# Performance work log

Hardware: AMD Instinct MI355X
Metric: run time of the kernel (lower is better)

The kernel has to match this reference:

```python
import jax, jax.numpy as jnp
import numpy as np
import math

B, S, T = 64, 512, 512
N, F_NODE, F_TRIP = 2000, 128, 128
D, H, GD = 512, 8, 64  # concat fusion: D == H*GD
SECONDS_PER_DAY = 3600.0 * 24.0


def cyclical_feat(t, mask):
    # t,[B,L]; mask,[B,L] -> [B,L,2]  (matches tf concat of sin/cos on axis 2)
    ang = 2.0 * math.pi * t / SECONDS_PER_DAY
    return jnp.stack([jnp.sin(ang) * mask, jnp.cos(ang) * mask], axis=-1)


def gat(x, adj, W, a_src, a_dst):
    # GAT-style AttentionAggregator, concat fusion + relu activation.
    # x:[N,F], adj:[N,N] (0/1), W:[H,F,G], a_src/a_dst:[H,G]
    h = jnp.einsum('nf,hfg->hng', x, W)                      # [H,N,G]
    es = jnp.einsum('hng,hg->hn', h, a_src)                  # [H,N]
    ed = jnp.einsum('hng,hg->hn', h, a_dst)                  # [H,N]
    e = jax.nn.leaky_relu(es[:, :, None] + ed[:, None, :], 0.2)  # [H,N,N]
    e = jnp.where(adj[None, :, :] > 0, e, -1e9)
    attn = jax.nn.softmax(e, axis=-1)                        # [H,N,N]
    out = jnp.einsum('hij,hjg->hig', attn, h)                # [H,N,G]
    out = jnp.transpose(out, (1, 0, 2)).reshape(x.shape[0], -1)  # [N,H*G]
    return jax.nn.relu(out)


def reconstruct_from_graph(graph_emb, index_array):
    # Vectorized equivalent of the TF TensorArray loop: indices are 1-based
    # with 0 = pad; valid entries are left-compacted, so masked gather == 
    # boolean_mask + gather + right-pad.
    valid = index_array > 0                                   # [B,S]
    idx = jnp.maximum(index_array - 1, 0)                     # [B,S]
    return jnp.where(valid[..., None], graph_emb[idx], 0.0)   # [B,S,D]


def setup_inputs() -> dict:
    key = jax.random.key(0)
    ks = jax.random.split(key, 13)
    region_batch = jax.random.normal(ks[0], (N, F_NODE), jnp.float32)
    trip_batch = jax.random.normal(ks[1], (B, T, F_TRIP), jnp.float32)
    len_r = jax.random.randint(ks[2], (B,), S // 2, S + 1)
    len_t = jax.random.randint(ks[3], (B,), T // 2, T + 1)
    region_mask = (jnp.arange(S)[None, :] < len_r[:, None]).astype(jnp.float32)
    trip_mask = (jnp.arange(T)[None, :] < len_t[:, None]).astype(jnp.float32)
    graph_mask = (jax.random.uniform(ks[4], (N, N)) < 0.02).astype(jnp.float32)
    graph_mask = jnp.maximum(graph_mask, jnp.eye(N, dtype=jnp.float32))  # self loops
    index_array = jax.random.randint(ks[5], (B, S), 1, N + 1).astype(jnp.int32)
    index_array = index_array * region_mask.astype(jnp.int32)  # 0 = pad (right side)
    arrive = jax.random.uniform(ks[6], (B, S), jnp.float32, 0.0, SECONDS_PER_DAY)
    depart = jax.random.uniform(ks[7], (B, T), jnp.float32, 0.0, SECONDS_PER_DAY)
    W_trip = jax.random.normal(ks[8], (F_TRIP, D), jnp.float32) * 0.05
    W_gat = jax.random.normal(ks[9], (H, F_NODE, GD), jnp.float32) * 0.05
    a_src = jax.random.normal(ks[10], (H, GD), jnp.float32) * 0.05
    a_dst = jax.random.normal(ks[11], (H, GD), jnp.float32) * 0.05
    W_time = jax.random.normal(ks[12], (2, D), jnp.float32) * 0.05
    b_time = jnp.zeros((D,), jnp.float32)
    return dict(region_batch=region_batch, trip_batch=trip_batch,
                trip_mask=trip_mask, region_mask=region_mask, graph_mask=graph_mask,
                arrive=arrive, depart=depart, index_array=index_array,
                W_trip=W_trip, W_gat=W_gat, a_src=a_src, a_dst=a_dst,
                W_time=W_time, b_time=b_time)


def reference(region_batch, trip_batch, trip_mask, region_mask, graph_mask,
              arrive, depart, index_array, W_trip, W_gat, a_src, a_dst,
              W_time, b_time):
    # FeatureExtractionLayer assumed Dense(no bias) + relu; dropout=0 (eval).
    trip_embeddings = jax.nn.relu(jnp.einsum('btf,fd->btd', trip_batch, W_trip))
    graph_embeddings = gat(region_batch, graph_mask, W_gat, a_src, a_dst)  # [N,D]
    region_embeddings = reconstruct_from_graph(graph_embeddings, index_array)
    arrive_feat = cyclical_feat(arrive, region_mask)   # [B,S,2]
    depart_feat = cyclical_feat(depart, trip_mask)     # [B,T,2]
    region_embeddings = region_embeddings + arrive_feat @ W_time + b_time
    trip_embeddings = trip_embeddings + depart_feat @ W_time + b_time
    return (region_embeddings, trip_embeddings)
```

## Files before the change

kernel.cpp:

```cpp
#include <hip/hip_runtime.h>
#include <hip/hip_bf16.h>

#define NB 2000
#define FN 128
#define DD 512
#define HH 8
#define GG 64
#define BB 64
#define SS 512
#define TT 512

__device__ __forceinline__ bool is_bf16(const void* graph_mask) {
    return (((const unsigned*)graph_mask)[0] & 0xFFFFu) == 0x3F80u;
}

template<bool BF>
__device__ __forceinline__ float ld(const void* p, long i) {
    if constexpr (BF) return __bfloat162float(((const __hip_bfloat16*)p)[i]);
    else              return ((const float*)p)[i];
}
template<bool BF>
__device__ __forceinline__ void st(void* p, long i, float v) {
    if constexpr (BF) ((__hip_bfloat16*)p)[i] = __float2bfloat16(v);
    else              ((float*)p)[i] = v;
}

template<bool BF>
__device__ __forceinline__ void ld4(const void* p, long i, float* o) {
    if constexpr (BF) {
        const unsigned short* q = (const unsigned short*)p + i;
        uint2 v = *reinterpret_cast<const uint2*>(q);
        o[0] = __uint_as_float((v.x & 0xFFFFu) << 16);
        o[1] = __uint_as_float((v.x >> 16) << 16);
        o[2] = __uint_as_float((v.y & 0xFFFFu) << 16);
        o[3] = __uint_as_float((v.y >> 16) << 16);
    } else {
        float4 a = *reinterpret_cast<const float4*>((const float*)p + i);
        o[0]=a.x; o[1]=a.y; o[2]=a.z; o[3]=a.w;
    }
}
template<bool BF>
__device__ __forceinline__ void ld8(const void* p, long i, float* o) {
    if constexpr (BF) {
        const unsigned short* q = (const unsigned short*)p + i;
        uint4 v = *reinterpret_cast<const uint4*>(q);
        unsigned a0 = v.x, a1 = v.y, a2 = v.z, a3 = v.w;
        o[0] = __uint_as_float((a0 & 0xFFFFu) << 16);
        o[1] = __uint_as_float((a0 >> 16) << 16);
        o[2] = __uint_as_float((a1 & 0xFFFFu) << 16);
        o[3] = __uint_as_float((a1 >> 16) << 16);
        o[4] = __uint_as_float((a2 & 0xFFFFu) << 16);
        o[5] = __uint_as_float((a2 >> 16) << 16);
        o[6] = __uint_as_float((a3 & 0xFFFFu) << 16);
        o[7] = __uint_as_float((a3 >> 16) << 16);
    } else {
        const float* q = (const float*)p + i;
        float4 a = *reinterpret_cast<const float4*>(q);
        float4 b = *reinterpret_cast<const float4*>(q + 4);
        o[0]=a.x; o[1]=a.y; o[2]=a.z; o[3]=a.w;
        o[4]=b.x; o[5]=b.y; o[6]=b.z; o[7]=b.w;
    }
}
__device__ __forceinline__ unsigned pack_bf2(float a, float b) {
    __hip_bfloat16 x = __float2bfloat16(a), y = __float2bfloat16(b);
    return (unsigned)*(unsigned short*)&x | ((unsigned)*(unsigned short*)&y << 16);
}
template<bool BF>
__device__ __forceinline__ void st8(void* p, long i, const float* v) {
    if constexpr (BF) {
        unsigned short* q = (unsigned short*)p + i;
        *reinterpret_cast<uint4*>(q) = make_uint4(
            pack_bf2(v[0], v[1]), pack_bf2(v[2], v[3]),
            pack_bf2(v[4], v[5]), pack_bf2(v[6], v[7]));
    } else {
        float* q = (float*)p + i;
        *reinterpret_cast<float4*>(q)     = make_float4(v[0],v[1],v[2],v[3]);
        *reinterpret_cast<float4*>(q + 4) = make_float4(v[4],v[5],v[6],v[7]);
    }
}

__device__ __forceinline__ unsigned short f2bf(float v) {
    __hip_bfloat16 h = __float2bfloat16(v);
    return *reinterpret_cast<unsigned short*>(&h);
}
__device__ __forceinline__ float bf2f(unsigned short s) {
    return __uint_as_float((unsigned)s << 16);
}

#define NPB 8

template<bool BF>
__device__ __forceinline__ void gat_h_body(
    const void* __restrict__ x, const void* __restrict__ Wg,
    const void* __restrict__ a_src, const void* __restrict__ a_dst,
    float* __restrict__ h_ws, float* __restrict__ es_ws, float* __restrict__ ed_ws,
    float (*__restrict__ xs)[FN])
{
    int n0  = blockIdx.x * NPB;
    int tid = threadIdx.x;
    int hh  = tid >> 5, gp = tid & 31;
    int g0  = gp * 2;

    if constexpr (BF) {
        for (int idx = tid; idx < NPB * FN / 8; idx += 256) {
            float o[8];
            ld8<BF>(x, (long)n0 * FN + idx * 8, o);
#pragma unroll
            for (int j = 0; j < 8; ++j) ((float*)xs)[idx * 8 + j] = o[j];
        }
    } else {
        const float4* src = (const float4*)((const float*)x + (long)n0 * FN);
        for (int idx = tid; idx < NPB * FN / 4; idx += 256)
            ((float4*)xs)[idx] = src[idx];
    }
    __syncthreads();

    float v0[NPB], v1[NPB];
#pragma unroll
    for (int nn = 0; nn < NPB; ++nn) { v0[nn] = 0.f; v1[nn] = 0.f; }

    if constexpr (BF) {
        const unsigned* wp = (const unsigned*)((const unsigned short*)Wg + (long)hh * FN * GG);
#pragma unroll 4
        for (int f = 0; f < FN; ++f) {
            unsigned w = wp[f * 32 + gp];
            float wx = __uint_as_float((w & 0xFFFFu) << 16);
            float wy = __uint_as_float((w >> 16) << 16);
#pragma unroll
            for (int nn = 0; nn < NPB; ++nn) {
                float xf = xs[nn][f];
                v0[nn] = fmaf(xf, wx, v0[nn]);
                v1[nn] = fmaf(xf, wy, v1[nn]);
            }
        }
    } else {
        const float2* wp = (const float2*)((const float*)Wg + (long)hh * FN * GG);
#pragma unroll 4
        for (int f = 0; f < FN; ++f) {
            float2 w = wp[f * 32 + gp];
#pragma unroll
            for (int nn = 0; nn < NPB; ++nn) {
                float xf = xs[nn][f];
                v0[nn] = fmaf(xf, w.x, v0[nn]);
                v1[nn] = fmaf(xf, w.y, v1[nn]);
            }
        }
    }

    float as0 = ld<BF>(a_src, hh * GG + g0), as1 = ld<BF>(a_src, hh * GG + g0 + 1);
    float ad0 = ld<BF>(a_dst, hh * GG + g0), ad1 = ld<BF>(a_dst, hh * GG + g0 + 1);
#pragma unroll
    for (int nn = 0; nn < NPB; ++nn) {
        int n = n0 + nn;
        *reinterpret_cast<float2*>(&h_ws[((long)hh * NB + n) * GG + g0]) =
            make_float2(v0[nn], v1[nn]);
        float s1 = v0[nn] * as0 + v1[nn] * as1;
        float s2 = v0[nn] * ad0 + v1[nn] * ad1;
        for (int off = 16; off > 0; off >>= 1) {
            s1 += __shfl_xor(s1, off);
            s2 += __shfl_xor(s2, off);
        }
        if (gp == 0) { es_ws[hh * NB + n] = s1; ed_ws[hh * NB + n] = s2; }
    }
}

__global__ __launch_bounds__(256) void gat_h_kernel(
    const void* x, const void* Wg, const void* a_src, const void* a_dst,
    float* h_ws, float* es_ws, float* ed_ws, const void* graph_mask)
{
    __shared__ float xs[NPB][FN];
    if (is_bf16(graph_mask)) gat_h_body<true >(x, Wg, a_src, a_dst, h_ws, es_ws, ed_ws, xs);
    else                     gat_h_body<false>(x, Wg, a_src, a_dst, h_ws, es_ws, ed_ws, xs);
}

#define ACAP 192

template<bool BF>
__device__ __forceinline__ void gat_attn_body(
    const void* __restrict__ adj,
    const float* __restrict__ h_ws, const float* __restrict__ es_ws,
    const float* __restrict__ ed_ws, float* __restrict__ ge_ws,
    int* __restrict__ jl, float (*__restrict__ wts)[ACAP],
    float* __restrict__ es_i, int* __restrict__ cnt)
{
    const int i    = blockIdx.x;
    const int tid  = threadIdx.x;
    const int w    = tid >> 6;
    const int lane = tid & 63;

    if (tid == 0) *cnt = 0;
    if (tid < HH) es_i[tid] = es_ws[tid * NB + i];
    __syncthreads();

    for (int base = w * 64; base < NB; base += 512) {
        int  j     = base + lane;
        bool valid = (j < NB) && (ld<BF>(adj, (long)i * NB + j) > 0.f);
        unsigned long long mask = __ballot(valid);
        int nv = __popcll(mask);
        int bs = 0;
        if (lane == 0 && nv) bs = atomicAdd(cnt, nv);
        bs = __shfl(bs, 0);
        if (valid) {
            int slot = bs + __popcll(mask & ((1ULL << lane) - 1ULL));
            jl[slot] = j;
        }
    }
    __syncthreads();
    const int cn = min(*cnt, ACAP);

    const float es = es_i[w];
    float e_r[3];
    float m = -INFINITY;
#pragma unroll
    for (int s = 0; s < 3; ++s) {
        int k = lane + s * 64;
        float e = -INFINITY;
        if (k < cn) {
            float ev = es + ed_ws[(long)w * NB + jl[k]];
            e = ev > 0.f ? ev : 0.2f * ev;
        }
        e_r[s] = e;
        m = fmaxf(m, e);
    }
    for (int off = 32; off > 0; off >>= 1) m = fmaxf(m, __shfl_xor(m, off));
    float l = 0.f;
#pragma unroll
    for (int s = 0; s < 3; ++s) {
        int k = lane + s * 64;
        if (k < cn) {
            float p = __expf(e_r[s] - m);
            wts[w][k] = p;
            l += p;
        }
    }
    for (int off = 32; off > 0; off >>= 1) l += __shfl_xor(l, off);

    const float* hp = h_ws + (long)w * NB * GG + lane;
    float acc = 0.f;
    int k = 0;
    for (; k + 4 <= cn; k += 4) {
        float e0 = wts[w][k],   e1 = wts[w][k+1];
        float e2 = wts[w][k+2], e3 = wts[w][k+3];
        int   j0 = jl[k],   j1 = jl[k+1], j2 = jl[k+2], j3 = jl[k+3];
        float h0 = hp[(long)j0 * GG];
        float h1 = hp[(long)j1 * GG];
        float h2 = hp[(long)j2 * GG];
        float h3 = hp[(long)j3 * GG];
        acc = fmaf(e3, h3, fmaf(e2, h2, fmaf(e1, h1, fmaf(e0, h0, acc))));
    }
    for (; k < cn; ++k)
        acc = fmaf(wts[w][k], hp[(long)jl[k] * GG], acc);

    ge_ws[(long)i * DD + w * GG + lane] = fmaxf(acc / l, 0.f);
}

__global__ __launch_bounds__(512) void gat_attn_kernel(
    const void* adj, const float* h_ws, const float* es_ws,
    const float* ed_ws, float* ge_ws)
{
    __shared__ int   jl[2048];
    __shared__ float wts[HH][ACAP];
    __shared__ float es_i[HH];
    __shared__ int   cnt;
    if (is_bf16(adj)) gat_attn_body<true >(adj, h_ws, es_ws, ed_ws, ge_ws, jl, wts, es_i, &cnt);
    else              gat_attn_body<false>(adj, h_ws, es_ws, ed_ws, ge_ws, jl, wts, es_i, &cnt);
}

template<bool BF>
__device__ __forceinline__ void region_out_body(
    const int* __restrict__ index_array, const void* __restrict__ arrive,
    const void* __restrict__ region_mask,
    const void* __restrict__ W_time, const void* __restrict__ b_time,
    const float* __restrict__ ge_ws, void* __restrict__ out)
{
    int row  = blockIdx.x * 4 + (threadIdx.x >> 6);
    int lane = threadIdx.x & 63;
    int d0   = lane * 8;
    int idx  = index_array[row];
    float mask = ld<BF>(region_mask, row);
    float t    = ld<BF>(arrive, row);
    float ang  = 6.28318530717958647692f * t / 86400.f;
    float sa = sinf(ang) * mask, ca = cosf(ang) * mask;
    float g[8] = {0.f,0.f,0.f,0.f,0.f,0.f,0.f,0.f};
    if (idx > 0) {
        const float* gp = ge_ws + (long)(idx - 1) * DD + d0;
        float4 a = *reinterpret_cast<const float4*>(gp);
        float4 b = *reinterpret_cast<const float4*>(gp + 4);
        g[0]=a.x; g[1]=a.y; g[2]=a.z; g[3]=a.w;
        g[4]=b.x; g[5]=b.y; g[6]=b.z; g[7]=b.w;
    }
    float wt0[8], wt1[8], bt[8], o[8];
    ld8<BF>(W_time, d0, wt0);
    ld8<BF>(W_time, DD + d0, wt1);
    ld8<BF>(b_time, d0, bt);
#pragma unroll
    for (int j = 0; j < 8; ++j)
        o[j] = g[j] + sa * wt0[j] + ca * wt1[j] + bt[j];
    st8<BF>(out, (long)row * DD + d0, o);
}

__global__ __launch_bounds__(256) void region_out_kernel(
    const int* index_array, const void* arrive, const void* region_mask,
    const void* W_time, const void* b_time, const float* ge_ws, void* out,
    const void* graph_mask)
{
    if (is_bf16(graph_mask))
        region_out_body<true >(index_array, arrive, region_mask, W_time, b_time, ge_ws, out);
    else
        region_out_body<false>(index_array, arrive, region_mask, W_time, b_time, ge_ws, out);
}

typedef __attribute__((ext_vector_type(8))) short bf16x8;
typedef __attribute__((ext_vector_type(4))) float f32x4;

#define MFMA_BF16 __builtin_amdgcn_mfma_f32_16x16x32_bf16

__global__ __launch_bounds__(256) void prep_x_kernel(
    const void* __restrict__ trip_batch, unsigned short* __restrict__ Xh_p,
    unsigned short* __restrict__ Xl_p, const void* graph_mask)
{
    if (is_bf16(graph_mask)) return;
    long i = ((long)blockIdx.x * 256 + threadIdx.x) * 8;
    const float* q = (const float*)trip_batch + i;
    float4 a = *reinterpret_cast<const float4*>(q);
    float4 b = *reinterpret_cast<const float4*>(q + 4);
    float v[8] = {a.x,a.y,a.z,a.w,b.x,b.y,b.z,b.w};
    unsigned short h[8], l[8];
#pragma unroll
    for (int j = 0; j < 8; ++j) {
        h[j] = f2bf(v[j]);
        l[j] = f2bf(v[j] - bf2f(h[j]));
    }
    *reinterpret_cast<uint4*>(Xh_p + i) = make_uint4(
        h[0] | ((unsigned)h[1] << 16), h[2] | ((unsigned)h[3] << 16),
        h[4] | ((unsigned)h[5] << 16), h[6] | ((unsigned)h[7] << 16));
    *reinterpret_cast<uint4*>(Xl_p + i) = make_uint4(
        l[0] | ((unsigned)l[1] << 16), l[2] | ((unsigned)l[3] << 16),
        l[4] | ((unsigned)l[5] << 16), l[6] | ((unsigned)l[7] << 16));
}

__global__ __launch_bounds__(256) void prep_w_kernel(
    const void* __restrict__ W_trip, unsigned short* __restrict__ Wh_p,
    unsigned short* __restrict__ Wl_p, const void* graph_mask)
{
    bool bf = is_bf16(graph_mask);
    int q  = blockIdx.x * 256 + threadIdx.x;
    int k  = q >> 7;
    int n0 = (q & 127) * 4;
    if (bf) {
        const unsigned short* w = (const unsigned short*)W_trip;
#pragma unroll
        for (int j = 0; j < 4; ++j)
            Wh_p[(n0 + j) * FN + k] = w[(long)k * DD + n0 + j];
    } else {
        float v[4];
        ld4<false>(W_trip, (long)k * DD + n0, v);
#pragma unroll
        for (int j = 0; j < 4; ++j) {
            unsigned short h = f2bf(v[j]);
            Wh_p[(n0 + j) * FN + k] = h;
            Wl_p[(n0 + j) * FN + k] = f2bf(v[j] - bf2f(h));
        }
    }
}

template<bool BF>
__device__ __forceinline__ void trip_gemm_body(
    const unsigned short* __restrict__ Xh_p, const unsigned short* __restrict__ Xl_p,
    const unsigned short* __restrict__ Wh_p, const unsigned short* __restrict__ Wl_p,
    const void* __restrict__ depart, const void* __restrict__ trip_mask,
    const void* __restrict__ W_time, const void* __restrict__ b_time,
    void* __restrict__ out,
    short* __restrict__ Xh, short* __restrict__ Xl,
    short* __restrict__ Wh, short* __restrict__ Wl)
{
    const int tid  = threadIdx.x;
    const int lane = tid & 63;
    const int wv   = tid >> 6;
    const int bx   = blockIdx.x & 7;
    const int by   = blockIdx.x >> 3;
    const int row0 = by * 64;
    const int c0   = bx * 64;

    f32x4 acc0 = {0.f,0.f,0.f,0.f}, acc1 = {0.f,0.f,0.f,0.f};
    f32x4 acc2 = {0.f,0.f,0.f,0.f}, acc3 = {0.f,0.f,0.f,0.f};

    const int mr  = wv * 16 + (lane & 15);
    const int nrb = lane & 15;
    const int kl  = (lane >> 4) * 8;

    for (int kh = 0; kh < 2; ++kh) {
        if (kh) __syncthreads();

        for (int q = tid; q < 512; q += 256) {
            int r  = q >> 3, k8 = q & 7;
            long src = (long)(row0 + r) * FN + kh * 64 + k8 * 8;
            int  dst = r * 64 + ((k8 * 8) ^ ((r & 7) << 3));
            *reinterpret_cast<uint4*>(&Xh[dst]) =
                *reinterpret_cast<const uint4*>(Xh_p + src);
            if constexpr (!BF)
                *reinterpret_cast<uint4*>(&Xl[dst]) =
                    *reinterpret_cast<const uint4*>(Xl_p + src);
        }
        for (int q = tid; q < 512; q += 256) {
            int n  = q >> 3, k8 = q & 7;
            long src = (long)(c0 + n) * FN + kh * 64 + k8 * 8;
            int  dst = n * 64 + ((k8 * 8) ^ ((n & 7) << 3));
            *reinterpret_cast<uint4*>(&Wh[dst]) =
                *reinterpret_cast<const uint4*>(Wh_p + src);
            if constexpr (!BF)
                *reinterpret_cast<uint4*>(&Wl[dst]) =
                    *reinterpret_cast<const uint4*>(Wl_p + src);
        }
        __syncthreads();

#pragma unroll
        for (int kc = 0; kc < 2; ++kc) {
            int k0 = kc * 32 + kl;
            int ax = mr * 64 + (k0 ^ ((mr & 7) << 3));
            bf16x8 ah = *reinterpret_cast<const bf16x8*>(&Xh[ax]);
            bf16x8 al;
            if constexpr (!BF) al = *reinterpret_cast<const bf16x8*>(&Xl[ax]);
#pragma unroll
            for (int nt = 0; nt < 4; ++nt) {
                int nr = nt * 16 + nrb, wi = nr * 64 + (k0 ^ ((nr & 7) << 3));
                bf16x8 bh = *reinterpret_cast<const bf16x8*>(&Wh[wi]);
                f32x4& acc = (nt == 0) ? acc0 : (nt == 1) ? acc1 : (nt == 2) ? acc2 : acc3;
                acc = MFMA_BF16(ah, bh, acc, 0, 0, 0);
                if constexpr (!BF) {
                    bf16x8 bl = *reinterpret_cast<const bf16x8*>(&Wl[wi]);
                    acc = MFMA_BF16(al, bh, acc, 0, 0, 0);
                    acc = MFMA_BF16(ah, bl, acc, 0, 0, 0);
                }
            }
        }
    }

    const int rbase = row0 + wv * 16 + (lane >> 4) * 4;
    float sa[4], ca[4];
#pragma unroll
    for (int r = 0; r < 4; ++r) {
        int   row  = rbase + r;
        float mask = ld<BF>(trip_mask, row);
        float t    = ld<BF>(depart, row);
        float ang  = 6.28318530717958647692f * t / 86400.f;
        sa[r] = sinf(ang) * mask;
        ca[r] = cosf(ang) * mask;
    }
    const long obase = (long)BB * SS * DD;
#pragma unroll
    for (int nt = 0; nt < 4; ++nt) {
        int   c   = c0 + nt * 16 + (lane & 15);
        float wt0 = ld<BF>(W_time, c);
        float wt1 = ld<BF>(W_time, DD + c);
        float bt  = ld<BF>(b_time, c);
        f32x4 a = (nt == 0) ? acc0 : (nt == 1) ? acc1 : (nt == 2) ? acc2 : acc3;
#pragma unroll
        for (int r = 0; r < 4; ++r) {
            float o = fmaxf(a[r], 0.f) + sa[r] * wt0 + ca[r] * wt1 + bt;
            st<BF>(out, obase + (long)(rbase + r) * DD + c, o);
        }
    }
}

__global__ __launch_bounds__(256) void trip_gemm_kernel(
    const void* trip_batch,
    const unsigned short* Xh_p, const unsigned short* Xl_p,
    const unsigned short* Wh_p, const unsigned short* Wl_p,
    const void* depart, const void* trip_mask,
    const void* W_time, const void* b_time, void* out, const void* graph_mask)
{
    __shared__ short Xh[64 * 64], Xl[64 * 64];
    __shared__ short Wh[64 * 64], Wl[64 * 64];
    if (is_bf16(graph_mask))
        trip_gemm_body<true >((const unsigned short*)trip_batch, Xl_p, Wh_p, Wl_p,
                              depart, trip_mask, W_time, b_time, out, Xh, Xl, Wh, Wl);
    else
        trip_gemm_body<false>(Xh_p, Xl_p, Wh_p, Wl_p,
                              depart, trip_mask, W_time, b_time, out, Xh, Xl, Wh, Wl);
}

template<bool BF>
__device__ __forceinline__ void trip_mfma_body(
    const void* __restrict__ trip_batch, const void* __restrict__ W_trip,
    const void* __restrict__ depart, const void* __restrict__ trip_mask,
    const void* __restrict__ W_time, const void* __restrict__ b_time,
    void* __restrict__ out,
    short* __restrict__ Xh, short* __restrict__ Xl,
    short* __restrict__ Wh, short* __restrict__ Wl)
{
    const int tid  = threadIdx.x;
    const int lane = tid & 63;
    const int wv   = tid >> 6;
    const int bx   = blockIdx.x & 7;
    const int by   = blockIdx.x >> 3;
    const int row0 = by * 64;
    const int c0   = bx * 64;

    f32x4 acc0 = {0.f,0.f,0.f,0.f}, acc1 = {0.f,0.f,0.f,0.f};
    f32x4 acc2 = {0.f,0.f,0.f,0.f}, acc3 = {0.f,0.f,0.f,0.f};

    const int mr  = wv * 16 + (lane & 15);
    const int nrb = lane & 15;
    const int kl  = (lane >> 4) * 8;

    for (int kh = 0; kh < 2; ++kh) {
        if (kh) __syncthreads();
        for (int q = tid; q < 1024; q += 256) {
            int r  = q >> 4;
            int k4 = (q & 15) * 4;
            float v[4];
            ld4<BF>(trip_batch, (long)(row0 + r) * FN + kh * 64 + k4, v);
            int base = r * 64 + (k4 ^ ((r & 7) << 3));
            ushort4 hs, ls;
            hs.x = f2bf(v[0]); ls.x = f2bf(v[0] - bf2f(hs.x));
            hs.y = f2bf(v[1]); ls.y = f2bf(v[1] - bf2f(hs.y));
            hs.z = f2bf(v[2]); ls.z = f2bf(v[2] - bf2f(hs.z));
            hs.w = f2bf(v[3]); ls.w = f2bf(v[3] - bf2f(hs.w));
            *reinterpret_cast<ushort4*>(&Xh[base]) = hs;
            *reinterpret_cast<ushort4*>(&Xl[base]) = ls;
        }
        for (int q = tid; q < 1024; q += 256) {
            int k  = q >> 4;
            int n0 = (q & 15) * 4;
            float v[4];
            ld4<BF>(W_trip, (long)(kh * 64 + k) * DD + c0 + n0, v);
#pragma unroll
            for (int j = 0; j < 4; ++j) {
                int n   = n0 + j;
                int idx = n * 64 + (k ^ ((n & 7) << 3));
                unsigned short h = f2bf(v[j]);
                Wh[idx] = (short)h;
                Wl[idx] = (short)f2bf(v[j] - bf2f(h));
            }
        }
        __syncthreads();

#pragma unroll
        for (int kc = 0; kc < 2; ++kc) {
            int k0 = kc * 32 + kl;
            int ax = mr * 64 + (k0 ^ ((mr & 7) << 3));
            bf16x8 ah = *reinterpret_cast<const bf16x8*>(&Xh[ax]);
            bf16x8 al = *reinterpret_cast<const bf16x8*>(&Xl[ax]);
#pragma unroll
            for (int nt = 0; nt < 4; ++nt) {
                int nr = nt * 16 + nrb, wi = nr * 64 + (k0 ^ ((nr & 7) << 3));
                bf16x8 bh = *reinterpret_cast<const bf16x8*>(&Wh[wi]);
                bf16x8 bl = *reinterpret_cast<const bf16x8*>(&Wl[wi]);
                f32x4& acc = (nt == 0) ? acc0 : (nt == 1) ? acc1 : (nt == 2) ? acc2 : acc3;
                acc = MFMA_BF16(ah, bh, acc, 0, 0, 0);
                acc = MFMA_BF16(al, bh, acc, 0, 0, 0);
                acc = MFMA_BF16(ah, bl, acc, 0, 0, 0);
            }
        }
    }

    const int rbase = row0 + wv * 16 + (lane >> 4) * 4;
    float sa[4], ca[4];
#pragma unroll
    for (int r = 0; r < 4; ++r) {
        int   row  = rbase + r;
        float mask = ld<BF>(trip_mask, row);
        float t    = ld<BF>(depart, row);
        float ang  = 6.28318530717958647692f * t / 86400.f;
        sa[r] = sinf(ang) * mask;
        ca[r] = cosf(ang) * mask;
    }
    const long obase = (long)BB * SS * DD;
#pragma unroll
    for (int nt = 0; nt < 4; ++nt) {
        int   c   = c0 + nt * 16 + (lane & 15);
        float wt0 = ld<BF>(W_time, c);
        float wt1 = ld<BF>(W_time, DD + c);
        float bt  = ld<BF>(b_time, c);
        f32x4 a = (nt == 0) ? acc0 : (nt == 1) ? acc1 : (nt == 2) ? acc2 : acc3;
#pragma unroll
        for (int r = 0; r < 4; ++r) {
            float o = fmaxf(a[r], 0.f) + sa[r] * wt0 + ca[r] * wt1 + bt;
            st<BF>(out, obase + (long)(rbase + r) * DD + c, o);
        }
    }
}

__global__ __launch_bounds__(256) void trip_out_kernel(
    const void* trip_batch, const void* W_trip, const void* depart,
    const void* trip_mask, const void* W_time, const void* b_time, void* out,
    const void* graph_mask)
{
    __shared__ short Xh[64 * 64], Xl[64 * 64];
    __shared__ short Wh[64 * 64], Wl[64 * 64];
    if (is_bf16(graph_mask))
        trip_mfma_body<true >(trip_batch, W_trip, depart, trip_mask, W_time, b_time, out, Xh, Xl, Wh, Wl);
    else
        trip_mfma_body<false>(trip_batch, W_trip, depart, trip_mask, W_time, b_time, out, Xh, Xl, Wh, Wl);
}

extern "C" void kernel_launch(void* const* d_in, const int* in_sizes, int n_in,
                              void* d_out, int out_size, void* d_ws, size_t ws_size,
                              hipStream_t stream) {
    const void* region_batch = d_in[0];
    const void* trip_batch   = d_in[1];
    const void* trip_mask    = d_in[2];
    const void* region_mask  = d_in[3];
    const void* graph_mask   = d_in[4];
    const void* arrive       = d_in[5];
    const void* depart       = d_in[6];
    const int*  index_array  = (const int*)d_in[7];
    const void* W_trip       = d_in[8];
    const void* W_gat        = d_in[9];
    const void* a_src        = d_in[10];
    const void* a_dst        = d_in[11];
    const void* W_time       = d_in[12];
    const void* b_time       = d_in[13];

    float* h_ws  = (float*)d_ws;
    float* es_ws = h_ws  + HH * NB * GG;
    float* ed_ws = es_ws + HH * NB;
    float* ge_ws = ed_ws + HH * NB;
    unsigned short* Xh_p = (unsigned short*)(ge_ws + (long)NB * DD);
    unsigned short* Xl_p = Xh_p + (long)BB * TT * FN;
    unsigned short* Wh_p = Xl_p + (long)BB * TT * FN;
    unsigned short* Wl_p = Wh_p + FN * DD;
    const size_t need = (size_t)((Wl_p + FN * DD) - (unsigned short*)d_ws) * 2;

    gat_h_kernel<<<NB / NPB, 256, 0, stream>>>(region_batch, W_gat, a_src, a_dst,
                                               h_ws, es_ws, ed_ws, graph_mask);
    gat_attn_kernel<<<NB, 512, 0, stream>>>(graph_mask, h_ws, es_ws, ed_ws, ge_ws);
    region_out_kernel<<<BB * SS / 4, 256, 0, stream>>>(index_array, arrive, region_mask,
                                                       W_time, b_time, ge_ws, d_out, graph_mask);
    if (ws_size >= need) {
        prep_x_kernel<<<(BB * TT * FN) / (256 * 8), 256, 0, stream>>>(
            trip_batch, Xh_p, Xl_p, graph_mask);
        prep_w_kernel<<<(FN * DD / 4) / 256, 256, 0, stream>>>(
            W_trip, Wh_p, Wl_p, graph_mask);
        trip_gemm_kernel<<<(BB * TT / 64) * (DD / 64), 256, 0, stream>>>(
            trip_batch, Xh_p, Xl_p, Wh_p, Wl_p,
            depart, trip_mask, W_time, b_time, d_out, graph_mask);
    } else {
        trip_out_kernel<<<(BB * TT / 64) * (DD / 64), 256, 0, stream>>>(
            trip_batch, W_trip, depart, trip_mask, W_time, b_time, d_out, graph_mask);
    }
}
```

Measured before the change: 269.8 us.

## Merge independent launches into combined front and tail kernels via block-range dispatch

Folds the GAT projection, the trip-input bf16 hi/lo split and the weight prep into one front kernel, with block index ranges choosing the role. The trip GEMM and the region gather/output are merged into one tail kernel in the same way, cutting six launches to three and letting independent work share the GPU. The adjacency scan in the attention kernel now issues all four row loads before doing the ballot compaction. The merged tail kernel reserves 32KB of LDS for every block, including the light region-output blocks, which may reduce their occupancy.

```diff
diff --git a/kernel.cpp b/kernel.cpp
--- a/kernel.cpp
+++ b/kernel.cpp
@@ -87,16 +87,21 @@
     return __uint_as_float((unsigned)s << 16);
 }
 
+typedef __attribute__((ext_vector_type(8))) short bf16x8;
+typedef __attribute__((ext_vector_type(4))) float f32x4;
+#define MFMA_BF16 __builtin_amdgcn_mfma_f32_16x16x32_bf16
+
 #define NPB 8
 
 template<bool BF>
 __device__ __forceinline__ void gat_h_body(
+    int blk,
     const void* __restrict__ x, const void* __restrict__ Wg,
     const void* __restrict__ a_src, const void* __restrict__ a_dst,
     float* __restrict__ h_ws, float* __restrict__ es_ws, float* __restrict__ ed_ws,
     float (*__restrict__ xs)[FN])
 {
-    int n0  = blockIdx.x * NPB;
+    int n0  = blk * NPB;
     int tid = threadIdx.x;
     int hh  = tid >> 5, gp = tid & 31;
     int g0  = gp * 2;
@@ -164,13 +169,75 @@
     }
 }
 
-__global__ __launch_bounds__(256) void gat_h_kernel(
-    const void* x, const void* Wg, const void* a_src, const void* a_dst,
-    float* h_ws, float* es_ws, float* ed_ws, const void* graph_mask)
+__device__ __forceinline__ void prep_x_body(
+    int blk, const void* __restrict__ trip_batch,
+    unsigned short* __restrict__ Xh_p, unsigned short* __restrict__ Xl_p)
+{
+    long i = ((long)blk * 256 + threadIdx.x) * 8;
+    const float* q = (const float*)trip_batch + i;
+    float4 a = *reinterpret_cast<const float4*>(q);
+    float4 b = *reinterpret_cast<const float4*>(q + 4);
+    float v[8] = {a.x,a.y,a.z,a.w,b.x,b.y,b.z,b.w};
+    unsigned short h[8], l[8];
+#pragma unroll
+    for (int j = 0; j < 8; ++j) {
+        h[j] = f2bf(v[j]);
+        l[j] = f2bf(v[j] - bf2f(h[j]));
+    }
+    *reinterpret_cast<uint4*>(Xh_p + i) = make_uint4(
+        h[0] | ((unsigned)h[1] << 16), h[2] | ((unsigned)h[3] << 16),
+        h[4] | ((unsigned)h[5] << 16), h[6] | ((unsigned)h[7] << 16));
+    *reinterpret_cast<uint4*>(Xl_p + i) = make_uint4(
+        l[0] | ((unsigned)l[1] << 16), l[2] | ((unsigned)l[3] << 16),
+        l[4] | ((unsigned)l[5] << 16), l[6] | ((unsigned)l[7] << 16));
+}
+
+__device__ __forceinline__ void prep_w_body(
+    int blk, bool bf, const void* __restrict__ W_trip,
+    unsigned short* __restrict__ Wh_p, unsigned short* __restrict__ Wl_p)
+{
+    int q  = blk * 256 + threadIdx.x;
+    int k  = q >> 7;
+    int n0 = (q & 127) * 4;
+    if (bf) {
+        const unsigned short* w = (const unsigned short*)W_trip;
+#pragma unroll
+        for (int j = 0; j < 4; ++j)
+            Wh_p[(n0 + j) * FN + k] = w[(long)k * DD + n0 + j];
+    } else {
+        float v[4];
+        ld4<false>(W_trip, (long)k * DD + n0, v);
+#pragma unroll
+        for (int j = 0; j < 4; ++j) {
+            unsigned short h = f2bf(v[j]);
+            Wh_p[(n0 + j) * FN + k] = h;
+            Wl_p[(n0 + j) * FN + k] = f2bf(v[j] - bf2f(h));
+        }
+    }
+}
+
+#define GATH_BLKS  (NB / NPB)
+#define PREPX_BLKS ((BB * TT * FN) / (256 * 8))
+#define PREPW_BLKS ((FN * DD / 4) / 256)
+
+__global__ __launch_bounds__(256) void front_kernel(
+    const void* region_batch, const void* Wg, const void* a_src, const void* a_dst,
+    float* h_ws, float* es_ws, float* ed_ws,
+    const void* trip_batch, unsigned short* Xh_p, unsigned short* Xl_p,
+    const void* W_trip, unsigned short* Wh_p, unsigned short* Wl_p,
+    const void* graph_mask)
 {
     __shared__ float xs[NPB][FN];
-    if (is_bf16(graph_mask)) gat_h_body<true >(x, Wg, a_src, a_dst, h_ws, es_ws, ed_ws, xs);
-    else                     gat_h_body<false>(x, Wg, a_src, a_dst, h_ws, es_ws, ed_ws, xs);
+    const bool bf  = is_bf16(graph_mask);
+    const int  bid = blockIdx.x;
+    if (bid < GATH_BLKS) {
+        if (bf) gat_h_body<true >(bid, region_batch, Wg, a_src, a_dst, h_ws, es_ws, ed_ws, xs);
+        else    gat_h_body<false>(bid, region_batch, Wg, a_src, a_dst, h_ws, es_ws, ed_ws, xs);
+    } else if (bid < GATH_BLKS + PREPX_BLKS) {
+        if (!bf) prep_x_body(bid - GATH_BLKS, trip_batch, Xh_p, Xl_p);
+    } else {
+        prep_w_body(bid - GATH_BLKS - PREPX_BLKS, bf, W_trip, Wh_p, Wl_p);
+    }
 }
 
 #define ACAP 192
@@ -192,18 +259,22 @@
     if (tid < HH) es_i[tid] = es_ws[tid * NB + i];
     __syncthreads();
 
-    for (int base = w * 64; base < NB; base += 512) {
-        int  j     = base + lane;
-        bool valid = (j < NB) && (ld<BF>(adj, (long)i * NB + j) > 0.f);
+    float av[4]; int jj[4];
+#pragma unroll
+    for (int s = 0; s < 4; ++s) {
+        int j = w * 64 + s * 512 + lane;
+        jj[s] = j;
+        av[s] = (j < NB) ? ld<BF>(adj, (long)i * NB + j) : 0.f;
+    }
+#pragma unroll
+    for (int s = 0; s < 4; ++s) {
+        bool valid = av[s] > 0.f;
         unsigned long long mask = __ballot(valid);
         int nv = __popcll(mask);
         int bs = 0;
         if (lane == 0 && nv) bs = atomicAdd(cnt, nv);
         bs = __shfl(bs, 0);
-        if (valid) {
-            int slot = bs + __popcll(mask & ((1ULL << lane) - 1ULL));
-            jl[slot] = j;
-        }
+        if (valid) jl[bs + __popcll(mask & ((1ULL << lane) - 1ULL))] = jj[s];
     }
     __syncthreads();
     const int cn = min(*cnt, ACAP);
@@ -268,12 +339,13 @@
 
 template<bool BF>
 __device__ __forceinline__ void region_out_body(
+    int blk,
     const int* __restrict__ index_array, const void* __restrict__ arrive,
     const void* __restrict__ region_mask,
     const void* __restrict__ W_time, const void* __restrict__ b_time,
     const float* __restrict__ ge_ws, void* __restrict__ out)
 {
-    int row  = blockIdx.x * 4 + (threadIdx.x >> 6);
+    int row  = blk * 4 + (threadIdx.x >> 6);
     int lane = threadIdx.x & 63;
     int d0   = lane * 8;
     int idx  = index_array[row];
@@ -305,67 +377,14 @@
     const void* graph_mask)
 {
     if (is_bf16(graph_mask))
-        region_out_body<true >(index_array, arrive, region_mask, W_time, b_time, ge_ws, out);
+        region_out_body<true >(blockIdx.x, index_array, arrive, region_mask, W_time, b_time, ge_ws, out);
     else
-        region_out_body<false>(index_array, arrive, region_mask, W_time, b_time, ge_ws, out);
-}
-
-typedef __attribute__((ext_vector_type(8))) short bf16x8;
-typedef __attribute__((ext_vector_type(4))) float f32x4;
-
-#define MFMA_BF16 __builtin_amdgcn_mfma_f32_16x16x32_bf16
-
-__global__ __launch_bounds__(256) void prep_x_kernel(
-    const void* __restrict__ trip_batch, unsigned short* __restrict__ Xh_p,
-    unsigned short* __restrict__ Xl_p, const void* graph_mask)
-{
-    if (is_bf16(graph_mask)) return;
-    long i = ((long)blockIdx.x * 256 + threadIdx.x) * 8;
-    const float* q = (const float*)trip_batch + i;
-    float4 a = *reinterpret_cast<const float4*>(q);
-    float4 b = *reinterpret_cast<const float4*>(q + 4);
-    float v[8] = {a.x,a.y,a.z,a.w,b.x,b.y,b.z,b.w};
-    unsigned short h[8], l[8];
-#pragma unroll
-    for (int j = 0; j < 8; ++j) {
-        h[j] = f2bf(v[j]);
-        l[j] = f2bf(v[j] - bf2f(h[j]));
-    }
-    *reinterpret_cast<uint4*>(Xh_p + i) = make_uint4(
-        h[0] | ((unsigned)h[1] << 16), h[2] | ((unsigned)h[3] << 16),
-        h[4] | ((unsigned)h[5] << 16), h[6] | ((unsigned)h[7] << 16));
-    *reinterpret_cast<uint4*>(Xl_p + i) = make_uint4(
-        l[0] | ((unsigned)l[1] << 16), l[2] | ((unsigned)l[3] << 16),
-        l[4] | ((unsigned)l[5] << 16), l[6] | ((unsigned)l[7] << 16));
-}
-
-__global__ __launch_bounds__(256) void prep_w_kernel(
-    const void* __restrict__ W_trip, unsigned short* __restrict__ Wh_p,
-    unsigned short* __restrict__ Wl_p, const void* graph_mask)
-{
-    bool bf = is_bf16(graph_mask);
-    int q  = blockIdx.x * 256 + threadIdx.x;
-    int k  = q >> 7;
-    int n0 = (q & 127) * 4;
-    if (bf) {
-        const unsigned short* w = (const unsigned short*)W_trip;
-#pragma unroll
-        for (int j = 0; j < 4; ++j)
-            Wh_p[(n0 + j) * FN + k] = w[(long)k * DD + n0 + j];
-    } else {
-        float v[4];
-        ld4<false>(W_trip, (long)k * DD + n0, v);
-#pragma unroll
-        for (int j = 0; j < 4; ++j) {
-            unsigned short h = f2bf(v[j]);
-            Wh_p[(n0 + j) * FN + k] = h;
-            Wl_p[(n0 + j) * FN + k] = f2bf(v[j] - bf2f(h));
-        }
-    }
+        region_out_body<false>(blockIdx.x, index_array, arrive, region_mask, W_time, b_time, ge_ws, out);
 }
 
 template<bool BF>
 __device__ __forceinline__ void trip_gemm_body(
+    int blk,
     const unsigned short* __restrict__ Xh_p, const unsigned short* __restrict__ Xl_p,
     const unsigned short* __restrict__ Wh_p, const unsigned short* __restrict__ Wl_p,
     const void* __restrict__ depart, const void* __restrict__ trip_mask,
@@ -377,8 +396,8 @@
     const int tid  = threadIdx.x;
     const int lane = tid & 63;
     const int wv   = tid >> 6;
-    const int bx   = blockIdx.x & 7;
-    const int by   = blockIdx.x >> 3;
+    const int bx   = blk & 7;
+    const int by   = blk >> 3;
     const int row0 = by * 64;
     const int c0   = bx * 64;
 
@@ -463,21 +482,45 @@
     }
 }
 
-__global__ __launch_bounds__(256) void trip_gemm_kernel(
+#define GEMM_BLKS ((BB * TT / 64) * (DD / 64))
+
+__global__ __launch_bounds__(256) void tail_kernel(
     const void* trip_batch,
     const unsigned short* Xh_p, const unsigned short* Xl_p,
     const unsigned short* Wh_p, const unsigned short* Wl_p,
     const void* depart, const void* trip_mask,
-    const void* W_time, const void* b_time, void* out, const void* graph_mask)
-{
-    __shared__ short Xh[64 * 64], Xl[64 * 64];
-    __shared__ short Wh[64 * 64], Wl[64 * 64];
-    if (is_bf16(graph_mask))
-        trip_gemm_body<true >((const unsigned short*)trip_batch, Xl_p, Wh_p, Wl_p,
-                              depart, trip_mask, W_time, b_time, out, Xh, Xl, Wh, Wl);
-    else
-        trip_gemm_body<false>(Xh_p, Xl_p, Wh_p, Wl_p,
-                              depart, trip_mask, W_time, b_time, out, Xh, Xl, Wh, Wl);
+    const int* index_array, const void* arrive, const void* region_mask,
+    const void* W_time, const void* b_time,
+    const float* ge_ws, void* out, const void* graph_mask)
+{
+    __shared__ short lds_s[4 * 64 * 64];
+    const bool bf  = is_bf16(graph_mask);
+    const int  bid = blockIdx.x;
+    if (bid < GEMM_BLKS) {
+        short* Xh = lds_s;
+        short* Xl = lds_s + 4096;
+        short* Wh = lds_s + 8192;
+        short* Wl = lds_s + 12288;
+        if (bf)
+            trip_gemm_body<true >(bid, (const unsigned short*)trip_batch, Xl_p, Wh_p, Wl_p,
+                                  depart, trip_mask, W_time, b_time, out, Xh, Xl, Wh, Wl);
+        else
+            trip_gemm_body<false>(bid, Xh_p, Xl_p, Wh_p, Wl_p,
+                                  depart, trip_mask, W_time, b_time, out, Xh, Xl, Wh, Wl);
+    } else {
+        int blk = bid - GEMM_BLKS;
+        if (bf) region_out_body<true >(blk, index_array, arrive, region_mask, W_time, b_time, ge_ws, out);
+        else    region_out_body<false>(blk, index_array, arrive, region_mask, W_time, b_time, ge_ws, out);
+    }
+}
+
+__global__ __launch_bounds__(256) void gat_h_kernel(
+    const void* x, const void* Wg, const void* a_src, const void* a_dst,
+    float* h_ws, float* es_ws, float* ed_ws, const void* graph_mask)
+{
+    __shared__ float xs[NPB][FN];
+    if (is_bf16(graph_mask)) gat_h_body<true >(blockIdx.x, x, Wg, a_src, a_dst, h_ws, es_ws, ed_ws, xs);
+    else                     gat_h_body<false>(blockIdx.x, x, Wg, a_src, a_dst, h_ws, es_ws, ed_ws, xs);
 }
 
 template<bool BF>
@@ -623,21 +666,21 @@
     unsigned short* Wl_p = Wh_p + FN * DD;
     const size_t need = (size_t)((Wl_p + FN * DD) - (unsigned short*)d_ws) * 2;
 
-    gat_h_kernel<<<NB / NPB, 256, 0, stream>>>(region_batch, W_gat, a_src, a_dst,
-                                               h_ws, es_ws, ed_ws, graph_mask);
-    gat_attn_kernel<<<NB, 512, 0, stream>>>(graph_mask, h_ws, es_ws, ed_ws, ge_ws);
-    region_out_kernel<<<BB * SS / 4, 256, 0, stream>>>(index_array, arrive, region_mask,
-                                                       W_time, b_time, ge_ws, d_out, graph_mask);
     if (ws_size >= need) {
-        prep_x_kernel<<<(BB * TT * FN) / (256 * 8), 256, 0, stream>>>(
-            trip_batch, Xh_p, Xl_p, graph_mask);
-        prep_w_kernel<<<(FN * DD / 4) / 256, 256, 0, stream>>>(
-            W_trip, Wh_p, Wl_p, graph_mask);
-        trip_gemm_kernel<<<(BB * TT / 64) * (DD / 64), 256, 0, stream>>>(
-            trip_batch, Xh_p, Xl_p, Wh_p, Wl_p,
-            depart, trip_mask, W_time, b_time, d_out, graph_mask);
-    } else {
-        trip_out_kernel<<<(BB * TT / 64) * (DD / 64), 256, 0, stream>>>(
+        front_kernel<<<GATH_BLKS + PREPX_BLKS + PREPW_BLKS, 256, 0, stream>>>(
+            region_batch, W_gat, a_src, a_dst, h_ws, es_ws, ed_ws,
+            trip_batch, Xh_p, Xl_p, W_trip, Wh_p, Wl_p, graph_mask);
+        gat_attn_kernel<<<NB, 512, 0, stream>>>(graph_mask, h_ws, es_ws, ed_ws, ge_ws);
+        tail_kernel<<<GEMM_BLKS + BB * SS / 4, 256, 0, stream>>>(
+            trip_batch, Xh_p, Xl_p, Wh_p, Wl_p, depart, trip_mask,
+            index_array, arrive, region_mask, W_time, b_time, ge_ws, d_out, graph_mask);
+    } else {
+        gat_h_kernel<<<GATH_BLKS, 256, 0, stream>>>(region_batch, W_gat, a_src, a_dst,
+                                                    h_ws, es_ws, ed_ws, graph_mask);
+        gat_attn_kernel<<<NB, 512, 0, stream>>>(graph_mask, h_ws, es_ws, ed_ws, ge_ws);
+        region_out_kernel<<<BB * SS / 4, 256, 0, stream>>>(index_array, arrive, region_mask,
+                                                           W_time, b_time, ge_ws, d_out, graph_mask);
+        trip_out_kernel<<<GEMM_BLKS, 256, 0, stream>>>(
             trip_batch, W_trip, depart, trip_mask, W_time, b_time, d_out, graph_mask);
     }
 }
```

Measured after the change: 268.1 us. About the same (-0.6%).
